# Optimization experiments

Measured on AMD Instinct MI355X. Metric: run time of the kernel, lower is better.

Reference implementation:

```python
import jax, jax.numpy as jnp
import numpy as np

B, T, IN, H = 1024, 128, 5, 100  # batch, seq_len, input_size, hidden_size


def setup_inputs() -> dict:
    key = jax.random.key(0)
    ks = jax.random.split(key, 20)
    bound = 1.0 / np.sqrt(H)  # PyTorch LSTM init: U(-1/sqrt(H), 1/sqrt(H))

    def u(k, shape):
        return jax.random.uniform(k, shape, jnp.float32, -bound, bound)

    inp = {"x": jax.random.normal(ks[0], (B, T, IN), jnp.float32)}
    i = 1
    for layer, din in [(0, IN), (1, 2 * H)]:
        for d in ("f", "b"):
            inp[f"w_ih_l{layer}{d}"] = u(ks[i], (4 * H, din)); i += 1
            inp[f"w_hh_l{layer}{d}"] = u(ks[i], (4 * H, H)); i += 1
            inp[f"b_ih_l{layer}{d}"] = u(ks[i], (4 * H,)); i += 1
            inp[f"b_hh_l{layer}{d}"] = u(ks[i], (4 * H,)); i += 1
    inp["fc_w"] = u(ks[17], (3, 2 * H))
    inp["fc_b"] = u(ks[18], (3,))
    return inp


def _run_dir(x, w_ih, w_hh, b_ih, b_hh, reverse):
    """One LSTM direction. x: [B,T,D] -> hidden seq [B,T,H]. PyTorch gate order i,f,g,o."""
    xT = jnp.swapaxes(x, 0, 1)  # [T,B,D]
    # precompute input contribution for all timesteps: [T,B,4H]
    xg = jnp.einsum('tbd,gd->tbg', xT, w_ih) + b_ih + b_hh

    def step(carry, g_in):
        h, c = carry
        g = g_in + h @ w_hh.T  # [B,4H]
        i, f, gg, o = jnp.split(g, 4, axis=-1)
        c = jax.nn.sigmoid(f) * c + jax.nn.sigmoid(i) * jnp.tanh(gg)
        h = jax.nn.sigmoid(o) * jnp.tanh(c)
        return (h, c), h

    b = x.shape[0]
    init = (jnp.zeros((b, H), x.dtype), jnp.zeros((b, H), x.dtype))
    _, hs = jax.lax.scan(step, init, xg, reverse=reverse)  # hs[t] aligned with time t
    return jnp.swapaxes(hs, 0, 1)  # [B,T,H]


def reference(x,
              w_ih_l0f, w_hh_l0f, b_ih_l0f, b_hh_l0f,
              w_ih_l0b, w_hh_l0b, b_ih_l0b, b_hh_l0b,
              w_ih_l1f, w_hh_l1f, b_ih_l1f, b_hh_l1f,
              w_ih_l1b, w_hh_l1b, b_ih_l1b, b_hh_l1b,
              fc_w, fc_b):
    # Layer 0 (bidirectional): [B,T,2H]
    h0 = jnp.concatenate([
        _run_dir(x, w_ih_l0f, w_hh_l0f, b_ih_l0f, b_hh_l0f, False),
        _run_dir(x, w_ih_l0b, w_hh_l0b, b_ih_l0b, b_hh_l0b, True),
    ], axis=-1)
    # (inter-layer dropout p=0.2 is identity in eval mode)
    # Layer 1 (bidirectional): [B,T,2H]
    h1 = jnp.concatenate([
        _run_dir(h0, w_ih_l1f, w_hh_l1f, b_ih_l1f, b_hh_l1f, False),
        _run_dir(h0, w_ih_l1b, w_hh_l1b, b_ih_l1b, b_hh_l1b, True),
    ], axis=-1)
    last = h1[:, -1, :]  # [B,2H]
    # (dropout p=0.5 is identity in eval mode)
    logits = last @ fc_w.T + fc_b  # [B,3]
    return jax.nn.softmax(logits, axis=1)
```

## Files before the change

### kernel.cpp

```cpp
#include <hip/hip_runtime.h>
#include <hip/hip_fp16.h>


typedef __attribute__((ext_vector_type(8))) short bf16x8;
typedef __attribute__((ext_vector_type(4))) float f32x4;

constexpr int Bsz = 1024, Tt = 128, IN_ = 5, H = 100, G = 400, D1 = 200;
constexpr int NP = 512;
constexpr int NT = 25;
constexpr int MB = 8;
constexpr int MB1 = 4;

__device__ __forceinline__ float sigm(float x)   { return 1.f / (1.f + __expf(-x)); }
__device__ __forceinline__ float tanhf_(float x) { return 1.f - 2.f / (__expf(2.f * x) + 1.f); }
__device__ __forceinline__ unsigned short f2bf(float f) {
  unsigned u = __float_as_uint(f);
  u += 0x7fff + ((u >> 16) & 1);
  return (unsigned short)(u >> 16);
}
__device__ __forceinline__ float partner8(float v) {
  return __uint_as_float(
      (unsigned)__builtin_amdgcn_ds_swizzle((int)__float_as_uint(v), 0x17));
}
__device__ __forceinline__ float partner4(float v) {
  return __uint_as_float(
      (unsigned)__builtin_amdgcn_ds_swizzle((int)__float_as_uint(v), 0x13));
}

__device__ __forceinline__ void pack_body(
    const float* wA, int KA, const float* wB, int KB, int kbo,
    const float* b1, const float* b2, int bias_k,
    unsigned short* dst, int Kg, int idx) {
  if (idx >= Kg * NP * 8) return;
  int jj = idx & 7, rest = idx >> 3;
  int np_ = rest % NP, g = rest / NP;
  int j = np_ >> 2, gate = np_ & 3;
  int k = g * 8 + jj;
  float v = 0.f;
  if (j < H) {
    int n = gate * H + j;
    if (k < KA) v = wA[n * KA + k];
    else if (KB > 0 && k >= kbo && k < kbo + KB) v = wB[n * KB + (k - kbo)];
    else if (k == bias_k) v = b1[n] + b2[n];
  }
  dst[idx] = f2bf(v);
}

__global__ void pack_all(
    const float* __restrict__ w_hh_l0f, const float* __restrict__ w_ih_l0f,
    const float* __restrict__ b_ih_l0f, const float* __restrict__ b_hh_l0f,
    const float* __restrict__ w_hh_l0b, const float* __restrict__ w_ih_l0b,
    const float* __restrict__ b_ih_l0b, const float* __restrict__ b_hh_l0b,
    const float* __restrict__ w_hh_l1f, const float* __restrict__ b_ih_l1f,
    const float* __restrict__ b_hh_l1f,
    const float* __restrict__ w_ih_l1f, const float* __restrict__ w_ih_l1b,
    const float* __restrict__ b_ih_l1b, const float* __restrict__ b_hh_l1b,
    unsigned short* __restrict__ pk0f, unsigned short* __restrict__ pk0b,
    unsigned short* __restrict__ pkhh, unsigned short* __restrict__ pkxg,
    unsigned short* __restrict__ pk1b) {
  int idx = blockIdx.x * 256 + threadIdx.x;
  switch (blockIdx.y) {
    case 0: pack_body(w_hh_l0f, 100, w_ih_l0f, 5, 100, b_ih_l0f, b_hh_l0f, 105, pk0f, 16, idx); break;
    case 1: pack_body(w_hh_l0b, 100, w_ih_l0b, 5, 100, b_ih_l0b, b_hh_l0b, 105, pk0b, 16, idx); break;
    case 2: pack_body(w_hh_l1f, 100, nullptr, 0, 0, b_ih_l1f, b_hh_l1f, -1, pkhh, 16, idx); break;
    case 3: pack_body(w_ih_l1f, 200, nullptr, 0, 0, b_ih_l1f, b_hh_l1f, 200, pkxg, 28, idx); break;
    default: pack_body(w_ih_l1b, 200, nullptr, 0, 0, b_ih_l1b, b_hh_l1b, 200, pk1b, 28, idx);
  }
}

__global__ __launch_bounds__(1024, 1) void lstm_l0(
    const float* __restrict__ x,
    const unsigned short* __restrict__ pk_f, const unsigned short* __restrict__ pk_b,
    unsigned short* __restrict__ h0fT, unsigned short* __restrict__ h0bT) {
  __shared__ __align__(16) short A_s[2][16][16][8];

  const int tid = threadIdx.x;
  const int lane = tid & 63, w = tid >> 6;
  const int q = lane >> 4, l16 = lane & 15;
  const int b0 = blockIdx.x * MB;
  const int dir = blockIdx.y;
  const unsigned short* pk = dir ? pk_b : pk_f;
  unsigned short* hT = dir ? h0bT : h0fT;

  for (int i = tid; i < 2 * 16 * 16 * 8; i += 1024) ((short*)A_s)[i] = 0;

  const int mtA = w, mtB = w + 16;
  const bool bvalid = (mtB < NT);
  bf16x8 wfA[4], wfB[4];
#pragma unroll
  for (int kt = 0; kt < 4; ++kt) {
    wfA[kt] = *(const bf16x8*)(pk + ((size_t)(kt * 4 + q) * NP + mtA * 16 + l16) * 8);
    wfB[kt] = *(const bf16x8*)(pk + ((size_t)(kt * 4 + q) * NP + mtB * 16 + l16) * 8);
  }
  float c = 0.f;
  const bool up = (l16 >= 8);
  const int mm = l16 & 7;
  const int j = (up ? mtB : mtA) * 4 + q;
  const bool valid = up ? bvalid : true;
  const int xm = tid / IN_, xe = tid - xm * IN_;
  const int sm = tid / 25, sj = (tid - (tid / 25) * 25) * 4;
  const float* xp = x + ((size_t)(b0 + xm) * Tt + (dir ? Tt - 2 : 1)) * IN_ + xe;
  const int xstride = dir ? -IN_ : IN_;
  unsigned short* hp =
      hT + ((size_t)(dir ? Tt - 1 : 0) * Bsz + b0 + sm) * H + sj;
  const int hstride = dir ? -(Bsz * H) : (Bsz * H);
  __syncthreads();
  if (tid < 16) {
    A_s[0][13][tid][1] = (short)f2bf(1.f);
    A_s[1][13][tid][1] = (short)f2bf(1.f);
  }
  if (tid < MB * IN_) {
    int t0 = dir ? (Tt - 1) : 0;
    int k = 100 + xe;
    A_s[0][k >> 3][xm][k & 7] =
        (short)f2bf(x[((size_t)(b0 + xm) * Tt + t0) * IN_ + xe]);
  }
  __syncthreads();

  int p = 0;
  for (int step = 0; step < Tt; ++step) {
    if (step > 0 && tid < 200) {
      uint2 hv = *(const uint2*)&A_s[p][sj >> 3][sm][sj & 7];
      *(uint2*)hp = hv;
      hp += hstride;
    }
    float xn = 0.f;
    const bool do_x = (tid < MB * IN_) && (step < Tt - 1);
    if (do_x) { xn = *xp; xp += xstride; }
    bf16x8 hfrag[4];
#pragma unroll
    for (int kt = 0; kt < 4; ++kt) hfrag[kt] = *(const bf16x8*)A_s[p][kt * 4 + q][l16];
    f32x4 accA = (f32x4){0.f, 0.f, 0.f, 0.f};
    f32x4 accB = (f32x4){0.f, 0.f, 0.f, 0.f};
#pragma unroll
    for (int kt = 0; kt < 4; ++kt)
      accA = __builtin_amdgcn_mfma_f32_16x16x32_bf16(wfA[kt], hfrag[kt], accA, 0, 0, 0);
    if (bvalid) {
#pragma unroll
      for (int kt = 0; kt < 4; ++kt)
        accB = __builtin_amdgcn_mfma_f32_16x16x32_bf16(wfB[kt], hfrag[kt], accB, 0, 0, 0);
    }
    float pb0 = partner8(accB[0]), pb1 = partner8(accB[1]);
    float pb2 = partner8(accB[2]), pb3 = partner8(accB[3]);
    float g0 = up ? pb0 : accA[0];
    float g1 = up ? pb1 : accA[1];
    float g2 = up ? pb2 : accA[2];
    float g3 = up ? pb3 : accA[3];
    float cc = sigm(g1) * c + sigm(g0) * tanhf_(g2);
    c = cc;
    float h = sigm(g3) * tanhf_(cc);
    if (valid) A_s[1 - p][j >> 3][mm][j & 7] = (short)f2bf(h);
    if (do_x) {
      int k = 100 + xe;
      A_s[1 - p][k >> 3][xm][k & 7] = (short)f2bf(xn);
    }
    __syncthreads();
    p ^= 1;
  }
  if (tid < 200) *(uint2*)hp = *(const uint2*)&A_s[p][sj >> 3][sm][sj & 7];
}

__global__ __launch_bounds__(1024, 1) void gemm_xg(
    const unsigned short* __restrict__ h0fT, const unsigned short* __restrict__ h0bT,
    const unsigned short* __restrict__ pkw, __half* __restrict__ xg) {
  __shared__ __align__(16) short B_s[28][64][8];
  const int tid = threadIdx.x;
  const int lane = tid & 63, w = tid >> 6;
  const int q = lane >> 4, l16 = lane & 15;
  const int r0 = blockIdx.x * 64;
  const size_t base = (size_t)r0 * H;

  for (int i = tid; i < 3 * 64 * 8; i += 1024) {
    int jj = i & 7, gl = i >> 9;
    ((short*)&B_s[25][0][0])[i] = (short)((gl == 0 && jj == 0) ? f2bf(1.f) : 0);
  }
  for (int idx = tid; idx < 1600; idx += 1024) {
    int m = idx / 25, j0 = (idx - (idx / 25) * 25) * 4;
    *(uint2*)&B_s[j0 >> 3][m][j0 & 7] = *(const uint2*)(h0fT + base + m * H + j0);
    int k = 100 + j0;
    *(uint2*)&B_s[k >> 3][m][k & 7] = *(const uint2*)(h0bT + base + m * H + j0);
  }

  const int mtA = w, mtB = w + 16;
  const bool bvalid = (mtB < NT);
  bf16x8 wfA[7], wfB[7];
#pragma unroll
  for (int kt = 0; kt < 7; ++kt) {
    wfA[kt] = *(const bf16x8*)(pkw + ((size_t)(kt * 4 + q) * NP + mtA * 16 + l16) * 8);
    wfB[kt] = *(const bf16x8*)(pkw + ((size_t)(kt * 4 + q) * NP + mtB * 16 + l16) * 8);
  }
  const int jA = mtA * 4 + q, jB = mtB * 4 + q;
  __syncthreads();

#pragma unroll
  for (int rg = 0; rg < 4; ++rg) {
    f32x4 accA = (f32x4){0.f, 0.f, 0.f, 0.f};
    f32x4 accB = (f32x4){0.f, 0.f, 0.f, 0.f};
#pragma unroll
    for (int kt = 0; kt < 7; ++kt) {
      bf16x8 hf = *(const bf16x8*)B_s[kt * 4 + q][rg * 16 + l16];
      accA = __builtin_amdgcn_mfma_f32_16x16x32_bf16(wfA[kt], hf, accA, 0, 0, 0);
      if (bvalid)
        accB = __builtin_amdgcn_mfma_f32_16x16x32_bf16(wfB[kt], hf, accB, 0, 0, 0);
    }
    const size_t row = (size_t)(r0 + rg * 16 + l16);
    {
      __half2 h01 = __floats2half2_rn(accA[0], accA[1]);
      __half2 h23 = __floats2half2_rn(accA[2], accA[3]);
      uint2 st; *(__half2*)&st.x = h01; *(__half2*)&st.y = h23;
      *(uint2*)(xg + row * G + 4 * jA) = st;
    }
    if (bvalid) {
      __half2 h01 = __floats2half2_rn(accB[0], accB[1]);
      __half2 h23 = __floats2half2_rn(accB[2], accB[3]);
      uint2 st; *(__half2*)&st.x = h01; *(__half2*)&st.y = h23;
      *(uint2*)(xg + row * G + 4 * jB) = st;
    }
  }
}

__global__ __launch_bounds__(1024, 1) void lstm_l1(
    const unsigned short* __restrict__ h0fT, const unsigned short* __restrict__ h0bT,
    const unsigned short* __restrict__ pk_hh, const unsigned short* __restrict__ pk1b,
    const __half* __restrict__ xg,
    const float* __restrict__ fc_w, const float* __restrict__ fc_b,
    float* __restrict__ out) {
  __shared__ __align__(16) short A_s[2][16][16][8];
  __shared__ __align__(16) short A2_s[28][16][8];
  __shared__ float hf_s[MB1][H];
  __shared__ float hb_s[MB1][H];
  __shared__ float fcw_s[3 * D1];
  __shared__ float fcb_s[3];
  __shared__ float logit_s[MB1][3];

  const int tid = threadIdx.x;
  const int lane = tid & 63, w = tid >> 6;
  const int q = lane >> 4, l16 = lane & 15;
  const int b0 = blockIdx.x * MB1;
  const uint2* xg2 = (const uint2*)xg;

  for (int i = tid; i < 2 * 16 * 16 * 8; i += 1024) ((short*)A_s)[i] = 0;
  for (int i = tid; i < 25 * 16 * 8; i += 1024) ((short*)A2_s)[i] = 0;
  for (int i = tid; i < 3 * 16 * 8; i += 1024) {
    int jj = i & 7, gl = i >> 7;
    ((short*)&A2_s[25][0][0])[i] = (short)((gl == 0 && jj == 0) ? f2bf(1.f) : 0);
  }
  for (int i = tid; i < 3 * D1; i += 1024) fcw_s[i] = fc_w[i];
  if (tid < 3) fcb_s[tid] = fc_b[tid];

  const bool busy = (w < 7);
  const int m = l16 & 3, g16 = l16 >> 2;
  const int myMt = w * 4 + g16;
  const int jme = myMt * 4 + q;
  const bool evalid = busy && (myMt < NT);
  int mts[4]; bool tv[4];
  bf16x8 wf[4][4];
  if (busy) {
#pragma unroll
    for (int i = 0; i < 4; ++i) {
      int mt = w * 4 + i; mts[i] = mt; tv[i] = (mt < NT);
#pragma unroll
      for (int kt = 0; kt < 4; ++kt)
        wf[i][kt] = *(const bf16x8*)(pk_hh + ((size_t)(kt * 4 + q) * NP + mt * 16 + l16) * 8);
    }
  }
  float c = 0.f;
  const uint2* xgp = xg2 + (size_t)(b0 + m) * 100 + jme;
  uint2 xgCur = {0, 0};
  if (busy) { xgCur = *xgp; xgp += Bsz * 100; }
  __syncthreads();

  int p = 0;
  for (int t = 0; t < Tt; ++t) {
    if (busy) {
      uint2 xgNxt = xgCur;
      if (t < Tt - 1) { xgNxt = *xgp; xgp += Bsz * 100; }
      bf16x8 hfrag[4];
#pragma unroll
      for (int kt = 0; kt < 4; ++kt) hfrag[kt] = *(const bf16x8*)A_s[p][kt * 4 + q][l16];
      f32x4 acc[4];
#pragma unroll
      for (int i = 0; i < 4; ++i) {
        acc[i] = (f32x4){0.f, 0.f, 0.f, 0.f};
        if (!tv[i]) continue;
#pragma unroll
        for (int kt = 0; kt < 4; ++kt)
          acc[i] = __builtin_amdgcn_mfma_f32_16x16x32_bf16(wf[i][kt], hfrag[kt], acc[i], 0, 0, 0);
      }
      float2 x01 = __half22float2(*(const __half2*)&xgCur.x);
      float2 x23 = __half22float2(*(const __half2*)&xgCur.y);
      float xr[4] = {x01.x, x01.y, x23.x, x23.y};
      float gr[4];
#pragma unroll
      for (int r = 0; r < 4; ++r) {
        float v0 = partner4(acc[0][r]);
        float v1 = partner4(acc[1][r]);
        float v2 = partner4(acc[2][r]);
        float v3 = partner4(acc[3][r]);
        float lo = (g16 & 1) ? v1 : v0;
        float hi = (g16 & 1) ? v3 : v2;
        gr[r] = ((g16 & 2) ? hi : lo) + xr[r];
      }
      float cc = sigm(gr[1]) * c + sigm(gr[0]) * tanhf_(gr[2]);
      c = cc;
      float h = sigm(gr[3]) * tanhf_(cc);
      if (evalid) {
        A_s[1 - p][jme >> 3][m][jme & 7] = (short)f2bf(h);
        if (t == Tt - 1) hf_s[m][jme] = h;
      }
      xgCur = xgNxt;
    }
    __syncthreads();
    p ^= 1;
  }

  {
    const size_t base = ((size_t)(Tt - 1) * Bsz + b0) * H;
    if (tid < 100) {
      int m2 = tid / 25, j0 = (tid - (tid / 25) * 25) * 4;
      *(uint2*)&A2_s[j0 >> 3][m2][j0 & 7] = *(const uint2*)(h0fT + base + m2 * H + j0);
      int k = 100 + j0;
      *(uint2*)&A2_s[k >> 3][m2][k & 7] = *(const uint2*)(h0bT + base + m2 * H + j0);
    }
  }
  __syncthreads();
  if (busy) {
    f32x4 acc[4];
#pragma unroll
    for (int i = 0; i < 4; ++i) acc[i] = (f32x4){0.f, 0.f, 0.f, 0.f};
#pragma unroll
    for (int kt = 0; kt < 7; ++kt) {
      bf16x8 hf = *(const bf16x8*)A2_s[kt * 4 + q][l16];
#pragma unroll
      for (int i = 0; i < 4; ++i) {
        if (!tv[i]) continue;
        bf16x8 wfb = *(const bf16x8*)(pk1b + ((size_t)(kt * 4 + q) * NP + mts[i] * 16 + l16) * 8);
        acc[i] = __builtin_amdgcn_mfma_f32_16x16x32_bf16(wfb, hf, acc[i], 0, 0, 0);
      }
    }
    float gr[4];
#pragma unroll
    for (int r = 0; r < 4; ++r) {
      float v0 = partner4(acc[0][r]);
      float v1 = partner4(acc[1][r]);
      float v2 = partner4(acc[2][r]);
      float v3 = partner4(acc[3][r]);
      float lo = (g16 & 1) ? v1 : v0;
      float hi = (g16 & 1) ? v3 : v2;
      gr[r] = (g16 & 2) ? hi : lo;
    }
    float cc = sigm(gr[0]) * tanhf_(gr[2]);
    if (evalid) hb_s[m][jme] = sigm(gr[3]) * tanhf_(cc);
  }
  __syncthreads();

  if (tid < MB1 * 3) {
    int mr = tid / 3, cls = tid - mr * 3;
    float s = fcb_s[cls];
    for (int jj = 0; jj < H; ++jj) s += fcw_s[cls * D1 + jj] * hf_s[mr][jj];
    for (int jj = 0; jj < H; ++jj) s += fcw_s[cls * D1 + H + jj] * hb_s[mr][jj];
    logit_s[mr][cls] = s;
  }
  __syncthreads();
  if (tid < MB1) {
    float a = logit_s[tid][0], b = logit_s[tid][1], cc = logit_s[tid][2];
    float mx = fmaxf(a, fmaxf(b, cc));
    float e0 = __expf(a - mx), e1 = __expf(b - mx), e2 = __expf(cc - mx);
    float inv = 1.f / (e0 + e1 + e2);
    out[(b0 + tid) * 3 + 0] = e0 * inv;
    out[(b0 + tid) * 3 + 1] = e1 * inv;
    out[(b0 + tid) * 3 + 2] = e2 * inv;
  }
}

extern "C" void kernel_launch(void* const* d_in, const int* in_sizes, int n_in,
                              void* d_out, int out_size, void* d_ws, size_t ws_size,
                              hipStream_t stream) {
  const float* x        = (const float*)d_in[0];
  const float* w_ih_l0f = (const float*)d_in[1];
  const float* w_hh_l0f = (const float*)d_in[2];
  const float* b_ih_l0f = (const float*)d_in[3];
  const float* b_hh_l0f = (const float*)d_in[4];
  const float* w_ih_l0b = (const float*)d_in[5];
  const float* w_hh_l0b = (const float*)d_in[6];
  const float* b_ih_l0b = (const float*)d_in[7];
  const float* b_hh_l0b = (const float*)d_in[8];
  const float* w_ih_l1f = (const float*)d_in[9];
  const float* w_hh_l1f = (const float*)d_in[10];
  const float* b_ih_l1f = (const float*)d_in[11];
  const float* b_hh_l1f = (const float*)d_in[12];
  const float* w_ih_l1b = (const float*)d_in[13];
  const float* b_ih_l1b = (const float*)d_in[15];
  const float* b_hh_l1b = (const float*)d_in[16];
  const float* fc_w     = (const float*)d_in[17];
  const float* fc_b     = (const float*)d_in[18];

  unsigned short* h0fT = (unsigned short*)d_ws;
  unsigned short* h0bT = h0fT + (size_t)Tt * Bsz * H;
  __half* xgT          = (__half*)(h0bT + (size_t)Tt * Bsz * H);
  unsigned short* pk0f = (unsigned short*)(xgT + (size_t)Tt * Bsz * G);
  unsigned short* pk0b = pk0f + 16 * NP * 8;
  unsigned short* pkhh = pk0b + 16 * NP * 8;
  unsigned short* pkxg = pkhh + 16 * NP * 8;
  unsigned short* pk1b = pkxg + 28 * NP * 8;

  pack_all<<<dim3(448, 5), 256, 0, stream>>>(
      w_hh_l0f, w_ih_l0f, b_ih_l0f, b_hh_l0f,
      w_hh_l0b, w_ih_l0b, b_ih_l0b, b_hh_l0b,
      w_hh_l1f, b_ih_l1f, b_hh_l1f,
      w_ih_l1f, w_ih_l1b, b_ih_l1b, b_hh_l1b,
      pk0f, pk0b, pkhh, pkxg, pk1b);

  lstm_l0<<<dim3(Bsz / MB, 2), 1024, 0, stream>>>(x, pk0f, pk0b, h0fT, h0bT);
  gemm_xg<<<(Bsz * Tt) / 64, 1024, 0, stream>>>(h0fT, h0bT, pkxg, xgT);
  lstm_l1<<<Bsz / MB1, 1024, 0, stream>>>(h0fT, h0bT, pkhh, pk1b, xgT,
                                          fc_w, fc_b, (float*)d_out);
}
```

Measured before the change: 376.2 us.

## Fuse layer-1 input projection GEMM into recurrent kernel using idle warps

Removes the separate gemm_xg kernel and its fp16 xg buffer in global memory. The idle warps (7-15) of lstm_l1 now compute the input-gate projection for upcoming timesteps into a triple-buffered shared-memory ring, prefetching h0 rows two steps ahead. The recurrent warps read xg from LDS in fp32 instead of streaming it from global memory. This cuts a large global write/read round trip and a kernel launch. The cost is extra MFMA work and register pressure inside the latency-bound recurrent loop, and more shared memory.

```diff
diff --git a/kernel.cpp b/kernel.cpp
--- a/kernel.cpp
+++ b/kernel.cpp
@@ -160,72 +160,15 @@
   if (tid < 200) *(uint2*)hp = *(const uint2*)&A_s[p][sj >> 3][sm][sj & 7];
 }
 
-__global__ __launch_bounds__(1024, 1) void gemm_xg(
-    const unsigned short* __restrict__ h0fT, const unsigned short* __restrict__ h0bT,
-    const unsigned short* __restrict__ pkw, __half* __restrict__ xg) {
-  __shared__ __align__(16) short B_s[28][64][8];
-  const int tid = threadIdx.x;
-  const int lane = tid & 63, w = tid >> 6;
-  const int q = lane >> 4, l16 = lane & 15;
-  const int r0 = blockIdx.x * 64;
-  const size_t base = (size_t)r0 * H;
-
-  for (int i = tid; i < 3 * 64 * 8; i += 1024) {
-    int jj = i & 7, gl = i >> 9;
-    ((short*)&B_s[25][0][0])[i] = (short)((gl == 0 && jj == 0) ? f2bf(1.f) : 0);
-  }
-  for (int idx = tid; idx < 1600; idx += 1024) {
-    int m = idx / 25, j0 = (idx - (idx / 25) * 25) * 4;
-    *(uint2*)&B_s[j0 >> 3][m][j0 & 7] = *(const uint2*)(h0fT + base + m * H + j0);
-    int k = 100 + j0;
-    *(uint2*)&B_s[k >> 3][m][k & 7] = *(const uint2*)(h0bT + base + m * H + j0);
-  }
-
-  const int mtA = w, mtB = w + 16;
-  const bool bvalid = (mtB < NT);
-  bf16x8 wfA[7], wfB[7];
-#pragma unroll
-  for (int kt = 0; kt < 7; ++kt) {
-    wfA[kt] = *(const bf16x8*)(pkw + ((size_t)(kt * 4 + q) * NP + mtA * 16 + l16) * 8);
-    wfB[kt] = *(const bf16x8*)(pkw + ((size_t)(kt * 4 + q) * NP + mtB * 16 + l16) * 8);
-  }
-  const int jA = mtA * 4 + q, jB = mtB * 4 + q;
-  __syncthreads();
-
-#pragma unroll
-  for (int rg = 0; rg < 4; ++rg) {
-    f32x4 accA = (f32x4){0.f, 0.f, 0.f, 0.f};
-    f32x4 accB = (f32x4){0.f, 0.f, 0.f, 0.f};
-#pragma unroll
-    for (int kt = 0; kt < 7; ++kt) {
-      bf16x8 hf = *(const bf16x8*)B_s[kt * 4 + q][rg * 16 + l16];
-      accA = __builtin_amdgcn_mfma_f32_16x16x32_bf16(wfA[kt], hf, accA, 0, 0, 0);
-      if (bvalid)
-        accB = __builtin_amdgcn_mfma_f32_16x16x32_bf16(wfB[kt], hf, accB, 0, 0, 0);
-    }
-    const size_t row = (size_t)(r0 + rg * 16 + l16);
-    {
-      __half2 h01 = __floats2half2_rn(accA[0], accA[1]);
-      __half2 h23 = __floats2half2_rn(accA[2], accA[3]);
-      uint2 st; *(__half2*)&st.x = h01; *(__half2*)&st.y = h23;
-      *(uint2*)(xg + row * G + 4 * jA) = st;
-    }
-    if (bvalid) {
-      __half2 h01 = __floats2half2_rn(accB[0], accB[1]);
-      __half2 h23 = __floats2half2_rn(accB[2], accB[3]);
-      uint2 st; *(__half2*)&st.x = h01; *(__half2*)&st.y = h23;
-      *(uint2*)(xg + row * G + 4 * jB) = st;
-    }
-  }
-}
-
 __global__ __launch_bounds__(1024, 1) void lstm_l1(
     const unsigned short* __restrict__ h0fT, const unsigned short* __restrict__ h0bT,
-    const unsigned short* __restrict__ pk_hh, const unsigned short* __restrict__ pk1b,
-    const __half* __restrict__ xg,
+    const unsigned short* __restrict__ pk_hh, const unsigned short* __restrict__ pkxg,
+    const unsigned short* __restrict__ pk1b,
     const float* __restrict__ fc_w, const float* __restrict__ fc_b,
     float* __restrict__ out) {
   __shared__ __align__(16) short A_s[2][16][16][8];
+  __shared__ __align__(16) short B2_s[2][28][16][8];
+  __shared__ __align__(16) float xgr[3 * 4 * 100 * 4];
   __shared__ __align__(16) short A2_s[28][16][8];
   __shared__ float hf_s[MB1][H];
   __shared__ float hb_s[MB1][H];
@@ -237,13 +180,17 @@
   const int lane = tid & 63, w = tid >> 6;
   const int q = lane >> 4, l16 = lane & 15;
   const int b0 = blockIdx.x * MB1;
-  const uint2* xg2 = (const uint2*)xg;
 
   for (int i = tid; i < 2 * 16 * 16 * 8; i += 1024) ((short*)A_s)[i] = 0;
   for (int i = tid; i < 25 * 16 * 8; i += 1024) ((short*)A2_s)[i] = 0;
   for (int i = tid; i < 3 * 16 * 8; i += 1024) {
     int jj = i & 7, gl = i >> 7;
     ((short*)&A2_s[25][0][0])[i] = (short)((gl == 0 && jj == 0) ? f2bf(1.f) : 0);
+  }
+  for (int i = tid; i < 2 * 3 * 16 * 8; i += 1024) {
+    int s = i / 384, off = i - s * 384;
+    ((short*)&B2_s[s][25][0][0])[off] =
+        (short)((off < 128 && (off & 7) == 0) ? f2bf(1.f) : 0);
   }
   for (int i = tid; i < 3 * D1; i += 1024) fcw_s[i] = fc_w[i];
   if (tid < 3) fcb_s[tid] = fc_b[tid];
@@ -265,16 +212,72 @@
     }
   }
   float c = 0.f;
-  const uint2* xgp = xg2 + (size_t)(b0 + m) * 100 + jme;
-  uint2 xgCur = {0, 0};
-  if (busy) { xgCur = *xgp; xgp += Bsz * 100; }
-  __syncthreads();
-
-  int p = 0;
+
+  const int gtid = tid - 448;
+  const bool gw = (w >= 7);
+  int xti[3]; bool xtv[3];
+  bf16x8 wx[3][7];
+  if (gw) {
+    int g = w - 7;
+#pragma unroll
+    for (int i = 0; i < 3; ++i) {
+      int ti = g * 3 + i; xti[i] = ti; xtv[i] = (ti < NT);
+#pragma unroll
+      for (int kt = 0; kt < 7; ++kt)
+        wx[i][kt] = *(const bf16x8*)(pkxg + ((size_t)(kt * 4 + q) * NP + ti * 16 + l16) * 8);
+    }
+  }
+  const bool ldr = gw && (gtid < 200);
+  const bool lf = (gtid < 100);
+  const int lr = lf ? gtid : (gtid - 100);
+  const int pm = lr / 25, pj = (lr - pm * 25) * 4;
+  const int dstk = lf ? pj : (100 + pj);
+  const unsigned short* hsrc = lf ? h0fT : h0bT;
+  const unsigned short* ph =
+      hsrc + ((size_t)3 * Bsz + b0 + pm) * H + pj;
+
+  if (tid < 400) {
+    int s = tid / 200, r = tid - s * 200;
+    bool f2 = (r < 100);
+    int r2 = f2 ? r : (r - 100);
+    int m2 = r2 / 25, j0 = (r2 - m2 * 25) * 4;
+    int k = f2 ? j0 : (100 + j0);
+    const unsigned short* src = f2 ? h0fT : h0bT;
+    *(uint2*)&B2_s[s][k >> 3][m2][k & 7] =
+        *(const uint2*)(src + ((size_t)s * Bsz + b0 + m2) * H + j0);
+  }
+  __syncthreads();
+  uint2 pre = {0, 0};
+  if (gw) {
+    if (ldr) pre = *(const uint2*)(hsrc + ((size_t)2 * Bsz + b0 + pm) * H + pj);
+#pragma unroll
+    for (int s = 0; s < 2; ++s) {
+      f32x4 acc[3];
+#pragma unroll
+      for (int i = 0; i < 3; ++i) {
+        acc[i] = (f32x4){0.f, 0.f, 0.f, 0.f};
+        if (!xtv[i]) continue;
+#pragma unroll
+        for (int kt = 0; kt < 7; ++kt) {
+          bf16x8 hf = *(const bf16x8*)B2_s[s][kt * 4 + q][l16];
+          acc[i] = __builtin_amdgcn_mfma_f32_16x16x32_bf16(wx[i][kt], hf, acc[i], 0, 0, 0);
+        }
+      }
+#pragma unroll
+      for (int i = 0; i < 3; ++i) {
+        if (xtv[i] && l16 < 4)
+          *(f32x4*)&xgr[((s * 4 + l16) * 100 + xti[i] * 4 + q) * 4] = acc[i];
+      }
+    }
+  }
+  __syncthreads();
+  if (ldr) *(uint2*)&B2_s[0][dstk >> 3][pm][dstk & 7] = pre;
+  __syncthreads();
+
+  int p = 0, s0 = 0, s2 = 2;
   for (int t = 0; t < Tt; ++t) {
     if (busy) {
-      uint2 xgNxt = xgCur;
-      if (t < Tt - 1) { xgNxt = *xgp; xgp += Bsz * 100; }
+      f32x4 xgv = *(const f32x4*)&xgr[((s0 * 4 + m) * 100 + jme) * 4];
       bf16x8 hfrag[4];
 #pragma unroll
       for (int kt = 0; kt < 4; ++kt) hfrag[kt] = *(const bf16x8*)A_s[p][kt * 4 + q][l16];
@@ -287,9 +290,6 @@
         for (int kt = 0; kt < 4; ++kt)
           acc[i] = __builtin_amdgcn_mfma_f32_16x16x32_bf16(wf[i][kt], hfrag[kt], acc[i], 0, 0, 0);
       }
-      float2 x01 = __half22float2(*(const __half2*)&xgCur.x);
-      float2 x23 = __half22float2(*(const __half2*)&xgCur.y);
-      float xr[4] = {x01.x, x01.y, x23.x, x23.y};
       float gr[4];
 #pragma unroll
       for (int r = 0; r < 4; ++r) {
@@ -299,7 +299,7 @@
         float v3 = partner4(acc[3][r]);
         float lo = (g16 & 1) ? v1 : v0;
         float hi = (g16 & 1) ? v3 : v2;
-        gr[r] = ((g16 & 2) ? hi : lo) + xr[r];
+        gr[r] = ((g16 & 2) ? hi : lo) + xgv[r];
       }
       float cc = sigm(gr[1]) * c + sigm(gr[0]) * tanhf_(gr[2]);
       c = cc;
@@ -308,10 +308,34 @@
         A_s[1 - p][jme >> 3][m][jme & 7] = (short)f2bf(h);
         if (t == Tt - 1) hf_s[m][jme] = h;
       }
-      xgCur = xgNxt;
+    } else {
+      const bool do_pf = (t < Tt - 3);
+      if (do_pf && ldr) { pre = *(const uint2*)ph; ph += Bsz * H; }
+      if (t < Tt - 2) {
+        f32x4 acc[3];
+#pragma unroll
+        for (int i = 0; i < 3; ++i) {
+          acc[i] = (f32x4){0.f, 0.f, 0.f, 0.f};
+          if (!xtv[i]) continue;
+#pragma unroll
+          for (int kt = 0; kt < 7; ++kt) {
+            bf16x8 hf = *(const bf16x8*)B2_s[t & 1][kt * 4 + q][l16];
+            acc[i] = __builtin_amdgcn_mfma_f32_16x16x32_bf16(wx[i][kt], hf, acc[i], 0, 0, 0);
+          }
+        }
+#pragma unroll
+        for (int i = 0; i < 3; ++i) {
+          if (xtv[i] && l16 < 4)
+            *(f32x4*)&xgr[((s2 * 4 + l16) * 100 + xti[i] * 4 + q) * 4] = acc[i];
+        }
+      }
+      if (do_pf && ldr)
+        *(uint2*)&B2_s[1 - (t & 1)][dstk >> 3][pm][dstk & 7] = pre;
     }
     __syncthreads();
     p ^= 1;
+    s0 = (s0 == 2) ? 0 : s0 + 1;
+    s2 = (s2 == 2) ? 0 : s2 + 1;
   }
 
   {
@@ -397,8 +421,7 @@
 
   unsigned short* h0fT = (unsigned short*)d_ws;
   unsigned short* h0bT = h0fT + (size_t)Tt * Bsz * H;
-  __half* xgT          = (__half*)(h0bT + (size_t)Tt * Bsz * H);
-  unsigned short* pk0f = (unsigned short*)(xgT + (size_t)Tt * Bsz * G);
+  unsigned short* pk0f = h0bT + (size_t)Tt * Bsz * H;
   unsigned short* pk0b = pk0f + 16 * NP * 8;
   unsigned short* pkhh = pk0b + 16 * NP * 8;
   unsigned short* pkxg = pkhh + 16 * NP * 8;
@@ -412,7 +435,6 @@
       pk0f, pk0b, pkhh, pkxg, pk1b);
 
   lstm_l0<<<dim3(Bsz / MB, 2), 1024, 0, stream>>>(x, pk0f, pk0b, h0fT, h0bT);
-  gemm_xg<<<(Bsz * Tt) / 64, 1024, 0, stream>>>(h0fT, h0bT, pkxg, xgT);
-  lstm_l1<<<Bsz / MB1, 1024, 0, stream>>>(h0fT, h0bT, pkhh, pk1b, xgT,
+  lstm_l1<<<Bsz / MB1, 1024, 0, stream>>>(h0fT, h0bT, pkhh, pkxg, pk1b,
                                           fc_w, fc_b, (float*)d_out);
 }
```

New measurement: 876.7 us. +133.0%, slower.
